# Optimization experiments

Measured on AMD Instinct MI355X. Metric: run time of the kernel, lower is better.

The kernel has to match this reference:

```python
import jax, jax.numpy as jnp
import numpy as np

RHO, MU, DT = 1.0, 0.1, 4.0
AX_X, AX_Y = -1, -2  # x = last axis, y = second-to-last


def first_derivative(f, ax, scheme):
    # unit grid spacing; boundary wrap is irrelevant since [1:-1,1:-1] is sliced off
    if scheme == 'left':
        return f - jnp.roll(f, 1, ax)
    if scheme == 'right':
        return jnp.roll(f, -1, ax) - f
    return 0.5 * (jnp.roll(f, -1, ax) - jnp.roll(f, 1, ax))  # central


def vel_map(f, ax, side):
    # staggered-grid interpolation of velocity to neighboring face
    if side == 'left':
        return 0.5 * (f + jnp.roll(f, 1, ax))
    return 0.5 * (f + jnp.roll(f, -1, ax))


def laplacian(f):
    return (jnp.roll(f, 1, AX_X) + jnp.roll(f, -1, AX_X)
            + jnp.roll(f, 1, AX_Y) + jnp.roll(f, -1, AX_Y) - 4.0 * f)


def setup_inputs() -> dict:
    key = jax.random.key(0)
    k1, k2, k3, k4 = jax.random.split(key, 4)
    B, H, W = 8, 1024, 1024
    return {
        'v_old': jax.random.normal(k1, (B, 2, H, W), dtype=jnp.float32),
        'v_new': jax.random.normal(k2, (B, 2, H, W), dtype=jnp.float32),
        'p_new': jax.random.normal(k3, (B, 1, H, W), dtype=jnp.float32),
        'flow_mask_mac': jax.random.randint(k4, (B, 1, H, W), 0, 2).astype(jnp.int32),
    }


def reference(v_old, v_new, p_new, flow_mask_mac):
    mask = flow_mask_mac.astype(v_old.dtype)
    v = 0.5 * (v_new + v_old)  # integration == 'imex'

    u_old, w_old = v_old[:, 0:1], v_old[:, 1:2]
    u_new, w_new = v_new[:, 0:1], v_new[:, 1:2]
    u, w = v[:, 0:1], v[:, 1:2]

    # x-momentum residual (channel 1)
    res_x = mask * (RHO * ((w_new - w_old) / DT
                           + w * first_derivative(w, AX_X, 'central')
                           + 0.5 * (vel_map(u, AX_X, 'left') * first_derivative(w, AX_Y, 'left')
                                    + vel_map(u, AX_X, 'right') * first_derivative(w, AX_Y, 'right')))
                    + first_derivative(p_new, AX_X, 'left')
                    - MU * laplacian(w))

    # y-momentum residual (channel 0)
    res_y = mask * (RHO * ((u_new - u_old) / DT
                           + u * first_derivative(u, AX_Y, 'central')
                           + 0.5 * (vel_map(w, AX_Y, 'left') * first_derivative(u, AX_X, 'left')
                                    + vel_map(w, AX_Y, 'right') * first_derivative(u, AX_X, 'right')))
                    + first_derivative(p_new, AX_Y, 'left')
                    - MU * laplacian(u))

    loss_x = jnp.mean(jnp.square(res_x)[:, :, 1:-1, 1:-1], axis=(1, 2, 3))
    loss_y = jnp.mean(jnp.square(res_y)[:, :, 1:-1, 1:-1], axis=(1, 2, 3))
    return loss_x + loss_y  # shape [B]
```

## Files before the change

### kernel.cpp

```cpp
#include <hip/hip_runtime.h>


#define NS_H 1024
#define NS_W 1024
#define RY   8
#define NBY  128
#define PARTS_PER_B NBY

__device__ __forceinline__ float4 ld4(const float* p) { return *(const float4*)p; }
__device__ __forceinline__ int4  ld4i(const int* p)   { return *(const int4*)p; }
__device__ __forceinline__ float4 avg4(float4 a, float4 b) {
    return make_float4(0.5f*(a.x+b.x), 0.5f*(a.y+b.y), 0.5f*(a.z+b.z), 0.5f*(a.w+b.w));
}
__device__ __forceinline__ float4 sub4(float4 a, float4 b) {
    return make_float4(a.x-b.x, a.y-b.y, a.z-b.z, a.w-b.w);
}

__global__ __launch_bounds__(256, 3) void ns_loss_partial(
    const float* __restrict__ v_old,
    const float* __restrict__ v_new,
    const float* __restrict__ p,
    const int*   __restrict__ mask,
    float* __restrict__ ws)
{
    const int blk = blockIdx.x;
    const int b   = blk / NBY;
    const int cy  = blk % NBY;
    const int y0  = 1 + cy * RY;
    const int ny  = min(RY, (NS_H - 1) - y0);

    const size_t hw = (size_t)NS_H * NS_W;
    const float* uo = v_old + (size_t)b * 2 * hw;
    const float* wo = uo + hw;
    const float* un = v_new + (size_t)b * 2 * hw;
    const float* wn = un + hw;
    const float* pb = p    + (size_t)b * hw;
    const int*   mb = mask + (size_t)b * hw;

    const int tid  = (int)threadIdx.x;
    const int lane = tid & 63;
    const int wid  = tid >> 6;
    const int x0   = tid * 4;

    __shared__ float edge[2][4][8];

    const int off_m = (y0 - 1) * NS_W + x0;
    const int off_c = off_m + NS_W;
    const int off_p = off_c + NS_W;

    float4 t0 = ld4(un + off_m), t1 = ld4(uo + off_m);
    float4 t2 = ld4(wn + off_m), t3 = ld4(wo + off_m);
    float4 t4 = ld4(un + off_c), t5 = ld4(uo + off_c);
    float4 t6 = ld4(wn + off_c), t7 = ld4(wo + off_c);
    float4 t8 = ld4(un + off_p), t9 = ld4(uo + off_p);
    float4 ta = ld4(wn + off_p), tb = ld4(wo + off_p);
    float4 p_m4 = ld4(pb + off_m);
    float4 p_c4 = ld4(pb + off_c);
    int4   m_c4 = ld4i(mb + off_c);

    const int offAv = (y0 + 2) * NS_W + x0, offAn = (y0 + 1) * NS_W + x0;
    const int offBv = (y0 + 3) * NS_W + x0, offBn = (y0 + 2) * NS_W + x0;
    float4 a_un = ld4(un + offAv), a_uo = ld4(uo + offAv);
    float4 a_wn = ld4(wn + offAv), a_wo = ld4(wo + offAv);
    float4 a_p  = ld4(pb + offAn); int4 a_m = ld4i(mb + offAn);
    float4 b_un = ld4(un + offBv), b_uo = ld4(uo + offBv);
    float4 b_wn = ld4(wn + offBv), b_wo = ld4(wo + offBv);
    float4 b_p  = ld4(pb + offBn); int4 b_m = ld4i(mb + offBn);

    float4 u_m = avg4(t0, t1), w_m = avg4(t2, t3);
    float4 u_c = avg4(t4, t5), du_c = sub4(t4, t5);
    float4 w_c = avg4(t6, t7), dw_c = sub4(t6, t7);
    float4 u_p = avg4(t8, t9), du_p = sub4(t8, t9);
    float4 w_p = avg4(ta, tb), dw_p = sub4(ta, tb);

    float acc = 0.f;

    auto iter = [&](int r, float4& g_un, float4& g_uo, float4& g_wn, float4& g_wo,
                    float4& g_p, int4& g_m) {
        const int y   = y0 + r;
        const int par = r & 1;

        if (lane == 63) {
            edge[par][wid][0] = u_c.w; edge[par][wid][1] = w_c.w; edge[par][wid][2] = p_c4.w;
        }
        if (lane == 0) {
            edge[par][wid][3] = u_c.x; edge[par][wid][4] = w_c.x;
        }
        __syncthreads();

        float ul = __shfl_up(u_c.w, 1), wl = __shfl_up(w_c.w, 1), pl = __shfl_up(p_c4.w, 1);
        if (lane == 0 && wid > 0) {
            ul = edge[par][wid-1][0]; wl = edge[par][wid-1][1]; pl = edge[par][wid-1][2];
        }
        float ur = __shfl_down(u_c.x, 1), wr = __shfl_down(w_c.x, 1);
        if (lane == 63 && wid < 3) {
            ur = edge[par][wid+1][3]; wr = edge[par][wid+1][4];
        }

        {
            const float uc[6]  = {ul, u_c.x, u_c.y, u_c.z, u_c.w, ur};
            const float wcv[6] = {wl, w_c.x, w_c.y, w_c.z, w_c.w, wr};
            const float uym[4] = {u_m.x, u_m.y, u_m.z, u_m.w};
            const float uyp[4] = {u_p.x, u_p.y, u_p.z, u_p.w};
            const float wym[4] = {w_m.x, w_m.y, w_m.z, w_m.w};
            const float wyp[4] = {w_p.x, w_p.y, w_p.z, w_p.w};
            const float du[4]  = {du_c.x, du_c.y, du_c.z, du_c.w};
            const float dw[4]  = {dw_c.x, dw_c.y, dw_c.z, dw_c.w};
            const float pcv[5] = {pl, p_c4.x, p_c4.y, p_c4.z, p_c4.w};
            const float pym[4] = {p_m4.x, p_m4.y, p_m4.z, p_m4.w};
            const int   mm[4]  = {m_c4.x, m_c4.y, m_c4.z, m_c4.w};

            #pragma unroll
            for (int j = 0; j < 4; ++j) {
                const int x = x0 + j;
                const float m = (x >= 1 && x <= NS_W - 2) ? (float)mm[j] : 0.f;
                const float u_cc = uc[j+1],  u_xm = uc[j],  u_xp = uc[j+2];
                const float w_cc = wcv[j+1], w_xm = wcv[j], w_xp = wcv[j+2];

                float res_x =
                    dw[j] * 0.25f
                  + w_cc * 0.5f * (w_xp - w_xm)
                  + 0.5f * ( 0.5f * (u_cc + u_xm) * (w_cc   - wym[j])
                           + 0.5f * (u_cc + u_xp) * (wyp[j] - w_cc  ) )
                  + (pcv[j+1] - pcv[j])
                  - 0.1f * (w_xm + w_xp + wym[j] + wyp[j] - 4.f * w_cc);

                float res_y =
                    du[j] * 0.25f
                  + u_cc * 0.5f * (uyp[j] - uym[j])
                  + 0.5f * ( 0.5f * (w_cc + wym[j]) * (u_cc - u_xm)
                           + 0.5f * (w_cc + wyp[j]) * (u_xp - u_cc) )
                  + (pcv[j+1] - pym[j])
                  - 0.1f * (u_xm + u_xp + uym[j] + uyp[j] - 4.f * u_cc);

                acc += m * (res_x * res_x + res_y * res_y);
            }
        }

        u_m = u_c;  w_m = w_c;
        u_c = u_p;  w_c = w_p;  du_c = du_p;  dw_c = dw_p;
        u_p = avg4(g_un, g_uo); du_p = sub4(g_un, g_uo);
        w_p = avg4(g_wn, g_wo); dw_p = sub4(g_wn, g_wo);
        p_m4 = p_c4; p_c4 = g_p; m_c4 = g_m;

        int rv = y + 4; if (rv > NS_H - 1) rv = NS_H - 1;
        int rn = y + 3; if (rn > NS_H - 1) rn = NS_H - 1;
        const int ov = rv * NS_W + x0;
        const int on = rn * NS_W + x0;
        g_un = ld4(un + ov); g_uo = ld4(uo + ov);
        g_wn = ld4(wn + ov); g_wo = ld4(wo + ov);
        g_p  = ld4(pb + on); g_m  = ld4i(mb + on);
    };

    for (int r = 0; r + 1 < ny; r += 2) {
        iter(r,     a_un, a_uo, a_wn, a_wo, a_p, a_m);
        iter(r + 1, b_un, b_uo, b_wn, b_wo, b_p, b_m);
    }

    #pragma unroll
    for (int off = 32; off > 0; off >>= 1)
        acc += __shfl_down(acc, off);

    __shared__ float smem[4];
    if (lane == 0) smem[wid] = acc;
    __syncthreads();

    if (tid == 0)
        ws[blk] = smem[0] + smem[1] + smem[2] + smem[3];
}

__global__ __launch_bounds__(256) void ns_loss_reduce(
    const float* __restrict__ ws, float* __restrict__ out)
{
    const int b = blockIdx.x;
    float acc = 0.f;
    for (int i = threadIdx.x; i < PARTS_PER_B; i += 256)
        acc += ws[b * PARTS_PER_B + i];

    #pragma unroll
    for (int off = 32; off > 0; off >>= 1)
        acc += __shfl_down(acc, off);

    __shared__ float smem[4];
    const int lane = threadIdx.x & 63;
    const int wid  = threadIdx.x >> 6;
    if (lane == 0) smem[wid] = acc;
    __syncthreads();

    if (threadIdx.x == 0) {
        const float inv = 1.0f / ((float)(NS_H - 2) * (float)(NS_W - 2));
        out[b] = (smem[0] + smem[1] + smem[2] + smem[3]) * inv;
    }
}

extern "C" void kernel_launch(void* const* d_in, const int* in_sizes, int n_in,
                              void* d_out, int out_size, void* d_ws, size_t ws_size,
                              hipStream_t stream) {
    const float* v_old = (const float*)d_in[0];
    const float* v_new = (const float*)d_in[1];
    const float* p_new = (const float*)d_in[2];
    const int*   msk   = (const int*)d_in[3];
    float* out = (float*)d_out;
    float* ws  = (float*)d_ws;

    const int B = out_size;

    ns_loss_partial<<<dim3(B * NBY), dim3(256), 0, stream>>>(v_old, v_new, p_new, msk, ws);
    ns_loss_reduce<<<dim3(B), dim3(256), 0, stream>>>(ws, out);
}
```

Measured before the change: 198.6 us.

## Load 4-row strip up front with single barrier and XCD-aware block remap

Each block now handles 4 rows instead of 8, doubling the block count. All six halo-inclusive rows are loaded at the start instead of streaming through a rolling register pipeline. Edge exchange happens through shared memory with one barrier rather than one per row. Block indices are permuted so consecutive blocks land on different XCDs while neighbouring strips share cache. The cost is more redundant halo reads (6 rows loaded per 4 computed instead of 10 per 8) and higher register pressure.

```diff
diff --git a/kernel.cpp b/kernel.cpp
--- a/kernel.cpp
+++ b/kernel.cpp
@@ -3,8 +3,8 @@
 
 #define NS_H 1024
 #define NS_W 1024
-#define RY   8
-#define NBY  128
+#define RPB 4
+#define NBY 256
 #define PARTS_PER_B NBY
 
 __device__ __forceinline__ float4 ld4(const float* p) { return *(const float4*)p; }
@@ -23,11 +23,12 @@
     const int*   __restrict__ mask,
     float* __restrict__ ws)
 {
-    const int blk = blockIdx.x;
-    const int b   = blk / NBY;
-    const int cy  = blk % NBY;
-    const int y0  = 1 + cy * RY;
-    const int ny  = min(RY, (NS_H - 1) - y0);
+    const int blkp = blockIdx.x;
+    const int lg   = (blkp & 7) * (NBY) + (blkp >> 3) % NBY + ((blkp >> 3) / NBY) * 0;
+    const int lg2  = (blkp & 7) * 256 + (blkp >> 3);
+    const int b    = lg2 / NBY;
+    const int cy   = lg2 % NBY;
+    const int y0   = 1 + cy * RPB;
 
     const size_t hw = (size_t)NS_H * NS_W;
     const float* uo = v_old + (size_t)b * 2 * hw;
@@ -41,120 +42,114 @@
     const int lane = tid & 63;
     const int wid  = tid >> 6;
     const int x0   = tid * 4;
-
-    __shared__ float edge[2][4][8];
-
-    const int off_m = (y0 - 1) * NS_W + x0;
-    const int off_c = off_m + NS_W;
-    const int off_p = off_c + NS_W;
-
-    float4 t0 = ld4(un + off_m), t1 = ld4(uo + off_m);
-    float4 t2 = ld4(wn + off_m), t3 = ld4(wo + off_m);
-    float4 t4 = ld4(un + off_c), t5 = ld4(uo + off_c);
-    float4 t6 = ld4(wn + off_c), t7 = ld4(wo + off_c);
-    float4 t8 = ld4(un + off_p), t9 = ld4(uo + off_p);
-    float4 ta = ld4(wn + off_p), tb = ld4(wo + off_p);
-    float4 p_m4 = ld4(pb + off_m);
-    float4 p_c4 = ld4(pb + off_c);
-    int4   m_c4 = ld4i(mb + off_c);
-
-    const int offAv = (y0 + 2) * NS_W + x0, offAn = (y0 + 1) * NS_W + x0;
-    const int offBv = (y0 + 3) * NS_W + x0, offBn = (y0 + 2) * NS_W + x0;
-    float4 a_un = ld4(un + offAv), a_uo = ld4(uo + offAv);
-    float4 a_wn = ld4(wn + offAv), a_wo = ld4(wo + offAv);
-    float4 a_p  = ld4(pb + offAn); int4 a_m = ld4i(mb + offAn);
-    float4 b_un = ld4(un + offBv), b_uo = ld4(uo + offBv);
-    float4 b_wn = ld4(wn + offBv), b_wo = ld4(wo + offBv);
-    float4 b_p  = ld4(pb + offBn); int4 b_m = ld4i(mb + offBn);
-
-    float4 u_m = avg4(t0, t1), w_m = avg4(t2, t3);
-    float4 u_c = avg4(t4, t5), du_c = sub4(t4, t5);
-    float4 w_c = avg4(t6, t7), dw_c = sub4(t6, t7);
-    float4 u_p = avg4(t8, t9), du_p = sub4(t8, t9);
-    float4 w_p = avg4(ta, tb), dw_p = sub4(ta, tb);
+    const bool has_r = (x0 + 4 < NS_W);
+
+    int R1 = y0,     R2 = y0 + 1, R3 = y0 + 2, R4 = y0 + 3, R5 = y0 + 4;
+    if (R3 > 1023) R3 = 1023;
+    if (R4 > 1023) R4 = 1023;
+    if (R5 > 1023) R5 = 1023;
+    const int o0 = (y0 - 1) * NS_W + x0;
+    const int o1 = R1 * NS_W + x0;
+    const int o2 = R2 * NS_W + x0;
+    const int o3 = R3 * NS_W + x0;
+    const int o4 = R4 * NS_W + x0;
+    const int o5 = R5 * NS_W + x0;
+
+    float4 un0 = ld4(un + o0), uo0 = ld4(uo + o0);
+    float4 un1 = ld4(un + o1), uo1 = ld4(uo + o1);
+    float4 un2 = ld4(un + o2), uo2 = ld4(uo + o2);
+    float4 un3 = ld4(un + o3), uo3 = ld4(uo + o3);
+    float4 un4 = ld4(un + o4), uo4 = ld4(uo + o4);
+    float4 un5 = ld4(un + o5), uo5 = ld4(uo + o5);
+    float4 wn0 = ld4(wn + o0), wo0 = ld4(wo + o0);
+    float4 wn1 = ld4(wn + o1), wo1 = ld4(wo + o1);
+    float4 wn2 = ld4(wn + o2), wo2 = ld4(wo + o2);
+    float4 wn3 = ld4(wn + o3), wo3 = ld4(wo + o3);
+    float4 wn4 = ld4(wn + o4), wo4 = ld4(wo + o4);
+    float4 wn5 = ld4(wn + o5), wo5 = ld4(wo + o5);
+    float4 P[5];
+    P[0] = ld4(pb + o0); P[1] = ld4(pb + o1); P[2] = ld4(pb + o2);
+    P[3] = ld4(pb + o3); P[4] = ld4(pb + o4);
+    int4 M[4];
+    M[0] = ld4i(mb + o1); M[1] = ld4i(mb + o2);
+    M[2] = ld4i(mb + o3); M[3] = ld4i(mb + o4);
+
+    float4 U[6], W[6], DU[4], DW[4];
+    U[0] = avg4(un0, uo0); W[0] = avg4(wn0, wo0);
+    U[1] = avg4(un1, uo1); W[1] = avg4(wn1, wo1); DU[0] = sub4(un1, uo1); DW[0] = sub4(wn1, wo1);
+    U[2] = avg4(un2, uo2); W[2] = avg4(wn2, wo2); DU[1] = sub4(un2, uo2); DW[1] = sub4(wn2, wo2);
+    U[3] = avg4(un3, uo3); W[3] = avg4(wn3, wo3); DU[2] = sub4(un3, uo3); DW[2] = sub4(wn3, wo3);
+    U[4] = avg4(un4, uo4); W[4] = avg4(wn4, wo4); DU[3] = sub4(un4, uo4); DW[3] = sub4(wn4, wo4);
+    U[5] = avg4(un5, uo5); W[5] = avg4(wn5, wo5);
+
+    __shared__ float edge[4][4][5];
+    if (lane == 63) {
+        #pragma unroll
+        for (int k = 0; k < 4; ++k) {
+            edge[wid][k][0] = U[k+1].w; edge[wid][k][1] = W[k+1].w; edge[wid][k][2] = P[k+1].w;
+        }
+    }
+    if (lane == 0) {
+        #pragma unroll
+        for (int k = 0; k < 4; ++k) {
+            edge[wid][k][3] = U[k+1].x; edge[wid][k][4] = W[k+1].x;
+        }
+    }
+    __syncthreads();
 
     float acc = 0.f;
 
-    auto iter = [&](int r, float4& g_un, float4& g_uo, float4& g_wn, float4& g_wo,
-                    float4& g_p, int4& g_m) {
-        const int y   = y0 + r;
-        const int par = r & 1;
-
-        if (lane == 63) {
-            edge[par][wid][0] = u_c.w; edge[par][wid][1] = w_c.w; edge[par][wid][2] = p_c4.w;
-        }
-        if (lane == 0) {
-            edge[par][wid][3] = u_c.x; edge[par][wid][4] = w_c.x;
-        }
-        __syncthreads();
-
-        float ul = __shfl_up(u_c.w, 1), wl = __shfl_up(w_c.w, 1), pl = __shfl_up(p_c4.w, 1);
+    #pragma unroll
+    for (int k = 0; k < 4; ++k) {
+        const float rowvalid = (y0 + k <= NS_H - 2) ? 1.f : 0.f;
+
+        float ul = __shfl_up(U[k+1].w, 1), wl = __shfl_up(W[k+1].w, 1), pl = __shfl_up(P[k+1].w, 1);
         if (lane == 0 && wid > 0) {
-            ul = edge[par][wid-1][0]; wl = edge[par][wid-1][1]; pl = edge[par][wid-1][2];
-        }
-        float ur = __shfl_down(u_c.x, 1), wr = __shfl_down(w_c.x, 1);
+            ul = edge[wid-1][k][0]; wl = edge[wid-1][k][1]; pl = edge[wid-1][k][2];
+        }
+        float ur = __shfl_down(U[k+1].x, 1), wr = __shfl_down(W[k+1].x, 1);
         if (lane == 63 && wid < 3) {
-            ur = edge[par][wid+1][3]; wr = edge[par][wid+1][4];
-        }
-
-        {
-            const float uc[6]  = {ul, u_c.x, u_c.y, u_c.z, u_c.w, ur};
-            const float wcv[6] = {wl, w_c.x, w_c.y, w_c.z, w_c.w, wr};
-            const float uym[4] = {u_m.x, u_m.y, u_m.z, u_m.w};
-            const float uyp[4] = {u_p.x, u_p.y, u_p.z, u_p.w};
-            const float wym[4] = {w_m.x, w_m.y, w_m.z, w_m.w};
-            const float wyp[4] = {w_p.x, w_p.y, w_p.z, w_p.w};
-            const float du[4]  = {du_c.x, du_c.y, du_c.z, du_c.w};
-            const float dw[4]  = {dw_c.x, dw_c.y, dw_c.z, dw_c.w};
-            const float pcv[5] = {pl, p_c4.x, p_c4.y, p_c4.z, p_c4.w};
-            const float pym[4] = {p_m4.x, p_m4.y, p_m4.z, p_m4.w};
-            const int   mm[4]  = {m_c4.x, m_c4.y, m_c4.z, m_c4.w};
-
-            #pragma unroll
-            for (int j = 0; j < 4; ++j) {
-                const int x = x0 + j;
-                const float m = (x >= 1 && x <= NS_W - 2) ? (float)mm[j] : 0.f;
-                const float u_cc = uc[j+1],  u_xm = uc[j],  u_xp = uc[j+2];
-                const float w_cc = wcv[j+1], w_xm = wcv[j], w_xp = wcv[j+2];
-
-                float res_x =
-                    dw[j] * 0.25f
-                  + w_cc * 0.5f * (w_xp - w_xm)
-                  + 0.5f * ( 0.5f * (u_cc + u_xm) * (w_cc   - wym[j])
-                           + 0.5f * (u_cc + u_xp) * (wyp[j] - w_cc  ) )
-                  + (pcv[j+1] - pcv[j])
-                  - 0.1f * (w_xm + w_xp + wym[j] + wyp[j] - 4.f * w_cc);
-
-                float res_y =
-                    du[j] * 0.25f
-                  + u_cc * 0.5f * (uyp[j] - uym[j])
-                  + 0.5f * ( 0.5f * (w_cc + wym[j]) * (u_cc - u_xm)
-                           + 0.5f * (w_cc + wyp[j]) * (u_xp - u_cc) )
-                  + (pcv[j+1] - pym[j])
-                  - 0.1f * (u_xm + u_xp + uym[j] + uyp[j] - 4.f * u_cc);
-
-                acc += m * (res_x * res_x + res_y * res_y);
-            }
-        }
-
-        u_m = u_c;  w_m = w_c;
-        u_c = u_p;  w_c = w_p;  du_c = du_p;  dw_c = dw_p;
-        u_p = avg4(g_un, g_uo); du_p = sub4(g_un, g_uo);
-        w_p = avg4(g_wn, g_wo); dw_p = sub4(g_wn, g_wo);
-        p_m4 = p_c4; p_c4 = g_p; m_c4 = g_m;
-
-        int rv = y + 4; if (rv > NS_H - 1) rv = NS_H - 1;
-        int rn = y + 3; if (rn > NS_H - 1) rn = NS_H - 1;
-        const int ov = rv * NS_W + x0;
-        const int on = rn * NS_W + x0;
-        g_un = ld4(un + ov); g_uo = ld4(uo + ov);
-        g_wn = ld4(wn + ov); g_wo = ld4(wo + ov);
-        g_p  = ld4(pb + on); g_m  = ld4i(mb + on);
-    };
-
-    for (int r = 0; r + 1 < ny; r += 2) {
-        iter(r,     a_un, a_uo, a_wn, a_wo, a_p, a_m);
-        iter(r + 1, b_un, b_uo, b_wn, b_wo, b_p, b_m);
+            ur = edge[wid+1][k][3]; wr = edge[wid+1][k][4];
+        }
+        if (!has_r) { ur = 0.f; wr = 0.f; }
+
+        const float uc[6]  = {ul, U[k+1].x, U[k+1].y, U[k+1].z, U[k+1].w, ur};
+        const float wcv[6] = {wl, W[k+1].x, W[k+1].y, W[k+1].z, W[k+1].w, wr};
+        const float uym[4] = {U[k].x, U[k].y, U[k].z, U[k].w};
+        const float uyp[4] = {U[k+2].x, U[k+2].y, U[k+2].z, U[k+2].w};
+        const float wym[4] = {W[k].x, W[k].y, W[k].z, W[k].w};
+        const float wyp[4] = {W[k+2].x, W[k+2].y, W[k+2].z, W[k+2].w};
+        const float du[4]  = {DU[k].x, DU[k].y, DU[k].z, DU[k].w};
+        const float dw[4]  = {DW[k].x, DW[k].y, DW[k].z, DW[k].w};
+        const float pcv[5] = {pl, P[k+1].x, P[k+1].y, P[k+1].z, P[k+1].w};
+        const float pym[4] = {P[k].x, P[k].y, P[k].z, P[k].w};
+        const int   mm[4]  = {M[k].x, M[k].y, M[k].z, M[k].w};
+
+        #pragma unroll
+        for (int j = 0; j < 4; ++j) {
+            const int x = x0 + j;
+            const float m = ((x >= 1 && x <= NS_W - 2) ? (float)mm[j] : 0.f) * rowvalid;
+            const float u_cc = uc[j+1],  u_xm = uc[j],  u_xp = uc[j+2];
+            const float w_cc = wcv[j+1], w_xm = wcv[j], w_xp = wcv[j+2];
+
+            float res_x =
+                dw[j] * 0.25f
+              + w_cc * 0.5f * (w_xp - w_xm)
+              + 0.5f * ( 0.5f * (u_cc + u_xm) * (w_cc   - wym[j])
+                       + 0.5f * (u_cc + u_xp) * (wyp[j] - w_cc  ) )
+              + (pcv[j+1] - pcv[j])
+              - 0.1f * (w_xm + w_xp + wym[j] + wyp[j] - 4.f * w_cc);
+
+            float res_y =
+                du[j] * 0.25f
+              + u_cc * 0.5f * (uyp[j] - uym[j])
+              + 0.5f * ( 0.5f * (w_cc + wym[j]) * (u_cc - u_xm)
+                       + 0.5f * (w_cc + wyp[j]) * (u_xp - u_cc) )
+              + (pcv[j+1] - pym[j])
+              - 0.1f * (u_xm + u_xp + uym[j] + uyp[j] - 4.f * u_cc);
+
+            acc += m * (res_x * res_x + res_y * res_y);
+        }
     }
 
     #pragma unroll
@@ -166,7 +161,7 @@
     __syncthreads();
 
     if (tid == 0)
-        ws[blk] = smem[0] + smem[1] + smem[2] + smem[3];
+        ws[lg2] = smem[0] + smem[1] + smem[2] + smem[3];
 }
 
 __global__ __launch_bounds__(256) void ns_loss_reduce(
```

New measurement: 212.9 us. 1.07x slower.

## Fuse final reduction via atomic counter, deepen row prefetch, relax barrier waits

Applied to the files above, without the earlier changes.

Merges the two-kernel partial/reduce scheme into one kernel: the last block to finish, found through an atomic counter, sums the per-block partials and writes the output. Row prefetch goes from two to three rows in flight, the 8-row loop is fully unrolled, and the barrier now waits only on LDS traffic so outstanding global loads stay in flight across it. Blocks are also remapped so consecutive block IDs interleave across batches. In exchange the launch adds a memset, and the row-validity mask and right-edge zeroing now handle boundary rows and columns explicitly.

```diff
diff --git a/kernel.cpp b/kernel.cpp
--- a/kernel.cpp
+++ b/kernel.cpp
@@ -5,7 +5,7 @@
 #define NS_W 1024
 #define RY   8
 #define NBY  128
-#define PARTS_PER_B NBY
+#define NBLK (8 * NBY)
 
 __device__ __forceinline__ float4 ld4(const float* p) { return *(const float4*)p; }
 __device__ __forceinline__ int4  ld4i(const int* p)   { return *(const int4*)p; }
@@ -16,18 +16,27 @@
     return make_float4(a.x-b.x, a.y-b.y, a.z-b.z, a.w-b.w);
 }
 
-__global__ __launch_bounds__(256, 3) void ns_loss_partial(
+__device__ __forceinline__ void barrier_keep_loads_inflight() {
+    __builtin_amdgcn_sched_barrier(0);
+    asm volatile("s_waitcnt lgkmcnt(0)" ::: "memory");
+    __builtin_amdgcn_s_barrier();
+    __builtin_amdgcn_sched_barrier(0);
+}
+
+__global__ __launch_bounds__(256, 3) void ns_loss_fused(
     const float* __restrict__ v_old,
     const float* __restrict__ v_new,
     const float* __restrict__ p,
     const int*   __restrict__ mask,
-    float* __restrict__ ws)
+    float* __restrict__ ws,
+    unsigned*   __restrict__ cnt,
+    float* __restrict__ out)
 {
-    const int blk = blockIdx.x;
-    const int b   = blk / NBY;
-    const int cy  = blk % NBY;
-    const int y0  = 1 + cy * RY;
-    const int ny  = min(RY, (NS_H - 1) - y0);
+    const int blkp = blockIdx.x;
+    const int lg   = (blkp & 7) * NBY + (blkp >> 3);
+    const int b    = lg / NBY;
+    const int cy   = lg % NBY;
+    const int y0   = 1 + cy * RY;
 
     const size_t hw = (size_t)NS_H * NS_W;
     const float* uo = v_old + (size_t)b * 2 * hw;
@@ -41,8 +50,9 @@
     const int lane = tid & 63;
     const int wid  = tid >> 6;
     const int x0   = tid * 4;
-
-    __shared__ float edge[2][4][8];
+    const bool has_r = (tid != 255);
+
+    __shared__ float edge[2][4][5];
 
     const int off_m = (y0 - 1) * NS_W + x0;
     const int off_c = off_m + NS_W;
@@ -58,14 +68,19 @@
     float4 p_c4 = ld4(pb + off_c);
     int4   m_c4 = ld4i(mb + off_c);
 
-    const int offAv = (y0 + 2) * NS_W + x0, offAn = (y0 + 1) * NS_W + x0;
-    const int offBv = (y0 + 3) * NS_W + x0, offBn = (y0 + 2) * NS_W + x0;
-    float4 a_un = ld4(un + offAv), a_uo = ld4(uo + offAv);
-    float4 a_wn = ld4(wn + offAv), a_wo = ld4(wo + offAv);
-    float4 a_p  = ld4(pb + offAn); int4 a_m = ld4i(mb + offAn);
-    float4 b_un = ld4(un + offBv), b_uo = ld4(uo + offBv);
-    float4 b_wn = ld4(wn + offBv), b_wo = ld4(wo + offBv);
-    float4 b_p  = ld4(pb + offBn); int4 b_m = ld4i(mb + offBn);
+    const int ov0 = (y0 + 2) * NS_W + x0, on0 = (y0 + 1) * NS_W + x0;
+    const int ov1 = (y0 + 3) * NS_W + x0, on1 = (y0 + 2) * NS_W + x0;
+    const int ov2 = (y0 + 4) * NS_W + x0, on2 = (y0 + 3) * NS_W + x0;
+    float4 a_un = ld4(un + ov0), a_uo = ld4(uo + ov0);
+    float4 a_wn = ld4(wn + ov0), a_wo = ld4(wo + ov0);
+    float4 a_p  = ld4(pb + on0); int4 a_m = ld4i(mb + on0);
+    float4 b_un = ld4(un + ov1), b_uo = ld4(uo + ov1);
+    float4 b_wn = ld4(wn + ov1), b_wo = ld4(wo + ov1);
+    float4 b_p  = ld4(pb + on1); int4 b_m = ld4i(mb + on1);
+    float4 c_un = ld4(un + ov2), c_uo = ld4(uo + ov2);
+    float4 c_wn = ld4(wn + ov2), c_wo = ld4(wo + ov2);
+    float4 c_p  = ld4(pb + on2); int4 c_m = ld4i(mb + on2);
+    __builtin_amdgcn_sched_barrier(0);
 
     float4 u_m = avg4(t0, t1), w_m = avg4(t2, t3);
     float4 u_c = avg4(t4, t5), du_c = sub4(t4, t5);
@@ -75,7 +90,8 @@
 
     float acc = 0.f;
 
-    auto iter = [&](int r, float4& g_un, float4& g_uo, float4& g_wn, float4& g_wo,
+    auto iter = [&](int r, bool consume, bool reissue,
+                    float4& g_un, float4& g_uo, float4& g_wn, float4& g_wo,
                     float4& g_p, int4& g_m) {
         const int y   = y0 + r;
         const int par = r & 1;
@@ -86,7 +102,7 @@
         if (lane == 0) {
             edge[par][wid][3] = u_c.x; edge[par][wid][4] = w_c.x;
         }
-        __syncthreads();
+        barrier_keep_loads_inflight();
 
         float ul = __shfl_up(u_c.w, 1), wl = __shfl_up(w_c.w, 1), pl = __shfl_up(p_c4.w, 1);
         if (lane == 0 && wid > 0) {
@@ -96,7 +112,9 @@
         if (lane == 63 && wid < 3) {
             ur = edge[par][wid+1][3]; wr = edge[par][wid+1][4];
         }
-
+        if (!has_r) { ur = 0.f; wr = 0.f; }
+
+        const float rowvalid = (y <= NS_H - 2) ? 1.f : 0.f;
         {
             const float uc[6]  = {ul, u_c.x, u_c.y, u_c.z, u_c.w, ur};
             const float wcv[6] = {wl, w_c.x, w_c.y, w_c.z, w_c.w, wr};
@@ -113,7 +131,7 @@
             #pragma unroll
             for (int j = 0; j < 4; ++j) {
                 const int x = x0 + j;
-                const float m = (x >= 1 && x <= NS_W - 2) ? (float)mm[j] : 0.f;
+                const float m = ((x >= 1 && x <= NS_W - 2) ? (float)mm[j] : 0.f) * rowvalid;
                 const float u_cc = uc[j+1],  u_xm = uc[j],  u_xp = uc[j+2];
                 const float w_cc = wcv[j+1], w_xm = wcv[j], w_xp = wcv[j+2];
 
@@ -137,25 +155,32 @@
             }
         }
 
-        u_m = u_c;  w_m = w_c;
-        u_c = u_p;  w_c = w_p;  du_c = du_p;  dw_c = dw_p;
-        u_p = avg4(g_un, g_uo); du_p = sub4(g_un, g_uo);
-        w_p = avg4(g_wn, g_wo); dw_p = sub4(g_wn, g_wo);
-        p_m4 = p_c4; p_c4 = g_p; m_c4 = g_m;
-
-        int rv = y + 4; if (rv > NS_H - 1) rv = NS_H - 1;
-        int rn = y + 3; if (rn > NS_H - 1) rn = NS_H - 1;
-        const int ov = rv * NS_W + x0;
-        const int on = rn * NS_W + x0;
-        g_un = ld4(un + ov); g_uo = ld4(uo + ov);
-        g_wn = ld4(wn + ov); g_wo = ld4(wo + ov);
-        g_p  = ld4(pb + on); g_m  = ld4i(mb + on);
+        if (consume) {
+            u_m = u_c;  w_m = w_c;
+            u_c = u_p;  w_c = w_p;  du_c = du_p;  dw_c = dw_p;
+            u_p = avg4(g_un, g_uo); du_p = sub4(g_un, g_uo);
+            w_p = avg4(g_wn, g_wo); dw_p = sub4(g_wn, g_wo);
+            p_m4 = p_c4; p_c4 = g_p; m_c4 = g_m;
+        }
+        if (reissue) {
+            int rv = y + 5; if (rv > NS_H - 1) rv = NS_H - 1;
+            int rn = y + 4; if (rn > NS_H - 1) rn = NS_H - 1;
+            const int ov = rv * NS_W + x0;
+            const int on = rn * NS_W + x0;
+            g_un = ld4(un + ov); g_uo = ld4(uo + ov);
+            g_wn = ld4(wn + ov); g_wo = ld4(wo + ov);
+            g_p  = ld4(pb + on); g_m  = ld4i(mb + on);
+        }
     };
 
-    for (int r = 0; r + 1 < ny; r += 2) {
-        iter(r,     a_un, a_uo, a_wn, a_wo, a_p, a_m);
-        iter(r + 1, b_un, b_uo, b_wn, b_wo, b_p, b_m);
-    }
+    iter(0, true,  true,  a_un, a_uo, a_wn, a_wo, a_p, a_m);
+    iter(1, true,  true,  b_un, b_uo, b_wn, b_wo, b_p, b_m);
+    iter(2, true,  true,  c_un, c_uo, c_wn, c_wo, c_p, c_m);
+    iter(3, true,  true,  a_un, a_uo, a_wn, a_wo, a_p, a_m);
+    iter(4, true,  false, b_un, b_uo, b_wn, b_wo, b_p, b_m);
+    iter(5, true,  false, c_un, c_uo, c_wn, c_wo, c_p, c_m);
+    iter(6, true,  false, a_un, a_uo, a_wn, a_wo, a_p, a_m);
+    iter(7, false, false, a_un, a_uo, a_wn, a_wo, a_p, a_m);
 
     #pragma unroll
     for (int off = 32; off > 0; off >>= 1)
@@ -166,30 +191,28 @@
     __syncthreads();
 
     if (tid == 0)
-        ws[blk] = smem[0] + smem[1] + smem[2] + smem[3];
-}
-
-__global__ __launch_bounds__(256) void ns_loss_reduce(
-    const float* __restrict__ ws, float* __restrict__ out)
-{
-    const int b = blockIdx.x;
-    float acc = 0.f;
-    for (int i = threadIdx.x; i < PARTS_PER_B; i += 256)
-        acc += ws[b * PARTS_PER_B + i];
-
-    #pragma unroll
-    for (int off = 32; off > 0; off >>= 1)
-        acc += __shfl_down(acc, off);
-
-    __shared__ float smem[4];
-    const int lane = threadIdx.x & 63;
-    const int wid  = threadIdx.x >> 6;
-    if (lane == 0) smem[wid] = acc;
+        ws[lg] = smem[0] + smem[1] + smem[2] + smem[3];
+
+    __threadfence();
+    __shared__ unsigned s_done;
+    if (tid == 0) {
+        unsigned old = atomicAdd(cnt, 1u);
+        s_done = (old == (unsigned)(NBLK - 1)) ? 1u : 0u;
+    }
     __syncthreads();
 
-    if (threadIdx.x == 0) {
+    if (s_done) {
+        __threadfence();
         const float inv = 1.0f / ((float)(NS_H - 2) * (float)(NS_W - 2));
-        out[b] = (smem[0] + smem[1] + smem[2] + smem[3]) * inv;
+        #pragma unroll
+        for (int bb = wid; bb < 8; bb += 4) {
+            float a = ws[bb * NBY + lane] + ws[bb * NBY + 64 + lane];
+            #pragma unroll
+            for (int off = 32; off > 0; off >>= 1)
+                a += __shfl_down(a, off);
+            if (lane == 0) out[bb] = a * inv;
+        }
+        if (tid == 0) *cnt = 0;
     }
 }
 
@@ -202,9 +225,9 @@
     const int*   msk   = (const int*)d_in[3];
     float* out = (float*)d_out;
     float* ws  = (float*)d_ws;
-
-    const int B = out_size;
-
-    ns_loss_partial<<<dim3(B * NBY), dim3(256), 0, stream>>>(v_old, v_new, p_new, msk, ws);
-    ns_loss_reduce<<<dim3(B), dim3(256), 0, stream>>>(ws, out);
-}
+    unsigned* cnt = (unsigned*)(ws + NBLK);
+
+    hipMemsetAsync(cnt, 0, sizeof(unsigned), stream);
+    ns_loss_fused<<<dim3(NBLK), dim3(256), 0, stream>>>(v_old, v_new, p_new, msk,
+                                                        ws, cnt, out);
+}
```

New measurement: 484.1 us. 144% more time.
